# Performance work log

Measured on AMD Instinct MI355X. Metric: run time of the kernel, lower is better.

## Reference

```python
import jax, jax.numpy as jnp
import numpy as np

N_NODES = 100000
N_EDGES = 3200000
D_IN = 256
D_OUT = 256


def setup_inputs() -> dict:
    key = jax.random.key(0)
    k1, k2, k3, k4, k5 = jax.random.split(key, 5)
    X = jax.random.normal(k1, (N_NODES, D_IN), dtype=jnp.float32)
    A_rows = jax.random.randint(k2, (N_EDGES,), 0, N_NODES, dtype=jnp.int64)
    A_cols = jax.random.randint(k3, (N_EDGES,), 0, N_NODES, dtype=jnp.int64)
    A_vals = jax.random.uniform(k4, (N_EDGES,), dtype=jnp.float32)
    # Xavier-uniform init of nn.Linear(in_dim, out_dim, bias=False): W is [out, in]
    limit = float(np.sqrt(6.0 / (D_IN + D_OUT)))
    W = jax.random.uniform(k5, (D_OUT, D_IN), minval=-limit, maxval=limit,
                           dtype=jnp.float32)
    return {"X": X, "A_rows": A_rows, "A_cols": A_cols, "A_vals": A_vals, "W": W}


def reference(X, A_rows, A_cols, A_vals, W):
    # AX = A_coo @ X : gather source features, scale by edge value, scatter-add by row
    msgs = X[A_cols] * A_vals[:, None]                  # [E, D_in]
    AX = jax.ops.segment_sum(msgs, A_rows, num_segments=N_NODES)  # [N, D_in]
    # Linear (bias=False) then ReLU; dropout p=0.0 is identity
    H = jax.nn.relu(AX @ W.T)                           # [N, D_out]
    return H
```

## Files before the change

### kernel.cpp

```cpp
#include <hip/hip_runtime.h>
#include <hip/hip_bf16.h>

#define N_NODES 100000
#define N_EDGES 3200000
#define D 256
#define SHIFT 9
#define NB 196
#define EPB 4096
#define NSPLIT 782
#define NGEMM 1563

typedef __attribute__((ext_vector_type(8))) short short8;
typedef __attribute__((ext_vector_type(4))) float f32x4;

__device__ inline short bfbits(float x) {
    __hip_bfloat16 h = __float2bfloat16(x);
    return __builtin_bit_cast(short, h);
}

__device__ inline short8 load_cvt8(const float* __restrict__ p) {
    float4 a = *(const float4*)p;
    float4 b = *(const float4*)(p + 4);
    short8 r;
    r[0] = bfbits(a.x); r[1] = bfbits(a.y); r[2] = bfbits(a.z); r[3] = bfbits(a.w);
    r[4] = bfbits(b.x); r[5] = bfbits(b.y); r[6] = bfbits(b.z); r[7] = bfbits(b.w);
    return r;
}

__device__ inline int block_excl_scan_256(int c, int* wsum, int& total) {
    const int lane = threadIdx.x & 63, wid = threadIdx.x >> 6;
    int v = c;
    #pragma unroll
    for (int off = 1; off < 64; off <<= 1) {
        int u = __shfl_up(v, off);
        if (lane >= off) v += u;
    }
    if (lane == 63) wsum[wid] = v;
    __syncthreads();
    int w0 = wsum[0], w1 = wsum[1], w2 = wsum[2], w3 = wsum[3];
    total = w0 + w1 + w2 + w3;
    int wex = (wid > 0 ? w0 : 0) + (wid > 1 ? w1 : 0) + (wid > 2 ? w2 : 0);
    return wex + v - c;
}

__global__ __launch_bounds__(256) void bucket_hist(
    const int* __restrict__ rows, int* __restrict__ gcnt, int nE)
{
    __shared__ int h[NB];
    for (int i = threadIdx.x; i < NB; i += 256) h[i] = 0;
    __syncthreads();
    for (int e = blockIdx.x * 256 + threadIdx.x; e < nE; e += gridDim.x * 256)
        atomicAdd(&h[rows[e] >> SHIFT], 1);
    __syncthreads();
    for (int i = threadIdx.x; i < NB; i += 256)
        if (h[i]) atomicAdd(&gcnt[i], h[i]);
}

__global__ __launch_bounds__(256) void bucket_scan(
    const int* __restrict__ gcnt, int* __restrict__ bbase,
    int* __restrict__ gcursor, int* __restrict__ row_ptr)
{
    __shared__ int wsum[4];
    int c = (threadIdx.x < NB) ? gcnt[threadIdx.x] : 0;
    int total;
    int ex = block_excl_scan_256(c, wsum, total);
    if (threadIdx.x < NB) { bbase[threadIdx.x] = ex; gcursor[threadIdx.x] = ex; }
    if (threadIdx.x == 0) { bbase[NB] = total; row_ptr[N_NODES] = total; }
}

__global__ __launch_bounds__(256) void split_gemm(
    const int* __restrict__ rows, const int* __restrict__ cols,
    const float* __restrict__ vals, int* __restrict__ gcursor,
    int2* __restrict__ bcv,
    const float* __restrict__ X, const float* __restrict__ W,
    unsigned short* __restrict__ Y, int nE)
{
    if (blockIdx.x < NSPLIT) {
        __shared__ int cnt[256];
        __shared__ int posp[256];
        const int t  = threadIdx.x;
        const int e0 = blockIdx.x * EPB;

        cnt[t] = 0;
        __syncthreads();

        int  myb[16];
        int2 mycv[16];
        #pragma unroll
        for (int k = 0; k < 16; ++k) {
            int e = e0 + k * 256 + t;
            if (e < nE) {
                int r = rows[e];
                myb[k]  = r >> SHIFT;
                mycv[k] = make_int2(((r & 511) << 17) | cols[e],
                                    __float_as_int(vals[e]));
                atomicAdd(&cnt[myb[k]], 1);
            } else {
                myb[k] = -1;
            }
        }
        __syncthreads();
        if (t < NB) {
            int c = cnt[t];
            posp[t] = c ? atomicAdd(&gcursor[t], c) : 0;
        }
        __syncthreads();
        #pragma unroll
        for (int k = 0; k < 16; ++k) {
            if (myb[k] >= 0) {
                int p = atomicAdd(&posp[myb[k]], 1);
                bcv[p] = mycv[k];
            }
        }
    } else {
        const int bid  = blockIdx.x - NSPLIT;
        const int wid  = threadIdx.x >> 6;
        const int lane = threadIdx.x & 63;
        const int m0   = bid * 64;
        const int n0   = wid * 64;
        const int lr   = lane & 15;
        const int ko   = (lane >> 4) * 8;
        const int M    = N_NODES;

        f32x4 acc[4][4] = {};

        #pragma unroll
        for (int k0 = 0; k0 < 256; k0 += 32) {
            short8 bfrag[4], afrag[4];
            #pragma unroll
            for (int j = 0; j < 4; ++j)
                bfrag[j] = load_cvt8(W + (size_t)(n0 + j * 16 + lr) * 256 + k0 + ko);
            #pragma unroll
            for (int i = 0; i < 4; ++i) {
                int r = m0 + i * 16 + lr;
                if (r > M - 1) r = M - 1;
                afrag[i] = load_cvt8(X + (size_t)r * 256 + k0 + ko);
            }
            #pragma unroll
            for (int i = 0; i < 4; ++i)
                #pragma unroll
                for (int j = 0; j < 4; ++j)
                    acc[i][j] = __builtin_amdgcn_mfma_f32_16x16x32_bf16(
                        afrag[i], bfrag[j], acc[i][j], 0, 0, 0);
        }

        #pragma unroll
        for (int i = 0; i < 4; ++i) {
            int rbase = m0 + i * 16 + (lane >> 4) * 4;
            #pragma unroll
            for (int rr = 0; rr < 4; ++rr) {
                int r = rbase + rr;
                if (r < M) {
                    #pragma unroll
                    for (int j = 0; j < 4; ++j)
                        Y[(size_t)r * 256 + n0 + j * 16 + lr] =
                            (unsigned short)bfbits(acc[i][j][rr]);
                }
            }
        }
    }
}

__global__ __launch_bounds__(256) void bucket_to_csr(
    const int* __restrict__ bbase, const int2* __restrict__ bcv,
    int* __restrict__ row_ptr, int2* __restrict__ cedge)
{
    __shared__ int hist[512];
    __shared__ int cur[512];
    __shared__ int wsum[4];
    const int t  = threadIdx.x;
    const int b  = blockIdx.x;
    const int r0 = b << SHIFT;
    const int s  = bbase[b], e = bbase[b + 1];

    hist[t] = 0; hist[t + 256] = 0;
    __syncthreads();
    for (int j = s + t; j < e; j += 256)
        atomicAdd(&hist[(unsigned)bcv[j].x >> 17], 1);
    __syncthreads();

    int c0 = hist[2 * t], c1 = hist[2 * t + 1];
    int total;
    int ex = block_excl_scan_256(c0 + c1, wsum, total);
    cur[2 * t]     = s + ex;
    cur[2 * t + 1] = s + ex + c0;
    int r = r0 + 2 * t;
    if (r     < N_NODES) row_ptr[r]     = s + ex;
    if (r + 1 < N_NODES) row_ptr[r + 1] = s + ex + c0;
    __syncthreads();

    for (int j = s + t; j < e; j += 256) {
        int2 q = bcv[j];
        int rl = (unsigned)q.x >> 17;
        int p = atomicAdd(&cur[rl], 1);
        cedge[p] = make_int2(q.x & 0x1FFFF, q.y);
    }
}

__global__ __launch_bounds__(256) void spmm_gather_relu(
    const unsigned short* __restrict__ Y,
    const int* __restrict__ row_ptr,
    const int2* __restrict__ cedge,
    float* __restrict__ H)
{
    int row  = blockIdx.x * 4 + (threadIdx.x >> 6);
    int lane = threadIdx.x & 63;
    if (row >= N_NODES) return;
    int s = row_ptr[row];
    int e = row_ptr[row + 1];

    float4 acc = make_float4(0.f, 0.f, 0.f, 0.f);
    const int fo = lane * 4;

    for (int base = s; base < e; base += 64) {
        int idx = base + lane;
        int2 q = make_int2(0, 0);
        if (idx < e) q = cedge[idx];
        int cnt = min(64, e - base);
        int j = 0;
        for (; j + 4 <= cnt; j += 4) {
            int c0 = __builtin_amdgcn_readfirstlane(__shfl(q.x, j));
            int c1 = __builtin_amdgcn_readfirstlane(__shfl(q.x, j + 1));
            int c2 = __builtin_amdgcn_readfirstlane(__shfl(q.x, j + 2));
            int c3 = __builtin_amdgcn_readfirstlane(__shfl(q.x, j + 3));
            float v0 = __int_as_float(__builtin_amdgcn_readfirstlane(__shfl(q.y, j)));
            float v1 = __int_as_float(__builtin_amdgcn_readfirstlane(__shfl(q.y, j + 1)));
            float v2 = __int_as_float(__builtin_amdgcn_readfirstlane(__shfl(q.y, j + 2)));
            float v3 = __int_as_float(__builtin_amdgcn_readfirstlane(__shfl(q.y, j + 3)));
            ushort4 y0 = *(const ushort4*)(Y + (size_t)c0 * 256 + fo);
            ushort4 y1 = *(const ushort4*)(Y + (size_t)c1 * 256 + fo);
            ushort4 y2 = *(const ushort4*)(Y + (size_t)c2 * 256 + fo);
            ushort4 y3 = *(const ushort4*)(Y + (size_t)c3 * 256 + fo);
            acc.x += __uint_as_float((unsigned)y0.x << 16) * v0;
            acc.y += __uint_as_float((unsigned)y0.y << 16) * v0;
            acc.z += __uint_as_float((unsigned)y0.z << 16) * v0;
            acc.w += __uint_as_float((unsigned)y0.w << 16) * v0;
            acc.x += __uint_as_float((unsigned)y1.x << 16) * v1;
            acc.y += __uint_as_float((unsigned)y1.y << 16) * v1;
            acc.z += __uint_as_float((unsigned)y1.z << 16) * v1;
            acc.w += __uint_as_float((unsigned)y1.w << 16) * v1;
            acc.x += __uint_as_float((unsigned)y2.x << 16) * v2;
            acc.y += __uint_as_float((unsigned)y2.y << 16) * v2;
            acc.z += __uint_as_float((unsigned)y2.z << 16) * v2;
            acc.w += __uint_as_float((unsigned)y2.w << 16) * v2;
            acc.x += __uint_as_float((unsigned)y3.x << 16) * v3;
            acc.y += __uint_as_float((unsigned)y3.y << 16) * v3;
            acc.z += __uint_as_float((unsigned)y3.z << 16) * v3;
            acc.w += __uint_as_float((unsigned)y3.w << 16) * v3;
        }
        for (; j < cnt; ++j) {
            int   cj = __builtin_amdgcn_readfirstlane(__shfl(q.x, j));
            float vj = __int_as_float(__builtin_amdgcn_readfirstlane(__shfl(q.y, j)));
            ushort4 y4 = *(const ushort4*)(Y + (size_t)cj * 256 + fo);
            acc.x += __uint_as_float((unsigned)y4.x << 16) * vj;
            acc.y += __uint_as_float((unsigned)y4.y << 16) * vj;
            acc.z += __uint_as_float((unsigned)y4.z << 16) * vj;
            acc.w += __uint_as_float((unsigned)y4.w << 16) * vj;
        }
    }
    float4 r;
    r.x = acc.x > 0.f ? acc.x : 0.f;
    r.y = acc.y > 0.f ? acc.y : 0.f;
    r.z = acc.z > 0.f ? acc.z : 0.f;
    r.w = acc.w > 0.f ? acc.w : 0.f;
    ((float4*)(H + (size_t)row * 256))[lane] = r;
}


extern "C" void kernel_launch(void* const* d_in, const int* in_sizes, int n_in,
                              void* d_out, int out_size, void* d_ws, size_t ws_size,
                              hipStream_t stream) {
    const float* X    = (const float*)d_in[0];
    const int*   rows = (const int*)d_in[1];
    const int*   cols = (const int*)d_in[2];
    const float* vals = (const float*)d_in[3];
    const float* W    = (const float*)d_in[4];
    float*       H    = (float*)d_out;

    char* ws = (char*)d_ws;
    unsigned short* Y       = (unsigned short*)(ws);
    int*            row_ptr = (int*)(ws + 51200000);
    int2*           cedge   = (int2*)(ws + 51600896);
    int2*           bcv     = (int2*)(ws + 77200896);
    int*            gcnt    = (int*)(ws + 102800896);
    int*            bbase   = (int*)(ws + 102801920);
    int*            gcursor = (int*)(ws + 102802944);

    hipMemsetAsync(gcnt, 0, NB * sizeof(int), stream);

    bucket_hist<<<256, 256, 0, stream>>>(rows, gcnt, N_EDGES);
    bucket_scan<<<1, 256, 0, stream>>>(gcnt, bbase, gcursor, row_ptr);
    split_gemm<<<NSPLIT + NGEMM, 256, 0, stream>>>(
        rows, cols, vals, gcursor, bcv, X, W, Y, N_EDGES);
    bucket_to_csr<<<NB, 256, 0, stream>>>(bbase, bcv, row_ptr, cedge);

    spmm_gather_relu<<<(N_NODES + 3) / 4, 256, 0, stream>>>(Y, row_ptr, cedge, H);
}
```

Measured before the change: 456.9 us.

## Replace histogram pass with fixed-capacity buckets and fuse CSR build into GEMM

New measurement: 411.0 us. 10.0% less time.

```diff
diff --git a/kernel.cpp b/kernel.cpp
--- a/kernel.cpp
+++ b/kernel.cpp
@@ -5,7 +5,8 @@
 #define N_EDGES 3200000
 #define D 256
 #define SHIFT 9
-#define NB 196
+#define NBC 196
+#define CAP 18000
 #define EPB 4096
 #define NSPLIT 782
 #define NGEMM 1563
@@ -43,77 +44,119 @@
     return wex + v - c;
 }
 
-__global__ __launch_bounds__(256) void bucket_hist(
-    const int* __restrict__ rows, int* __restrict__ gcnt, int nE)
-{
-    __shared__ int h[NB];
-    for (int i = threadIdx.x; i < NB; i += 256) h[i] = 0;
-    __syncthreads();
-    for (int e = blockIdx.x * 256 + threadIdx.x; e < nE; e += gridDim.x * 256)
-        atomicAdd(&h[rows[e] >> SHIFT], 1);
-    __syncthreads();
-    for (int i = threadIdx.x; i < NB; i += 256)
-        if (h[i]) atomicAdd(&gcnt[i], h[i]);
-}
-
-__global__ __launch_bounds__(256) void bucket_scan(
-    const int* __restrict__ gcnt, int* __restrict__ bbase,
-    int* __restrict__ gcursor, int* __restrict__ row_ptr)
-{
+__global__ __launch_bounds__(256) void init_cursor(int* __restrict__ gcursor)
+{
+    int t = threadIdx.x;
+    if (t < NBC) gcursor[t] = t * CAP;
+}
+
+__global__ __launch_bounds__(256) void bucket_split(
+    const int* __restrict__ rows, const int* __restrict__ cols,
+    const float* __restrict__ vals, int* __restrict__ gcursor,
+    int2* __restrict__ bcv, int nE)
+{
+    __shared__ int cnt[256];
+    __shared__ int startp[256];
+    __shared__ int posp[256];
+    __shared__ int gb[256];
     __shared__ int wsum[4];
-    int c = (threadIdx.x < NB) ? gcnt[threadIdx.x] : 0;
+    __shared__ int2 scv[EPB];
+    const int t  = threadIdx.x;
+    const int e0 = blockIdx.x * EPB;
+
+    cnt[t] = 0;
+    __syncthreads();
+
+    int  myb[16];
+    int2 mycv[16];
+    #pragma unroll
+    for (int k = 0; k < 16; ++k) {
+        int e = e0 + k * 256 + t;
+        if (e < nE) {
+            int r = rows[e];
+            myb[k]  = r >> SHIFT;
+            mycv[k] = make_int2(((r & 511) << 17) | cols[e],
+                                __float_as_int(vals[e]));
+            atomicAdd(&cnt[myb[k]], 1);
+        } else {
+            myb[k] = -1;
+        }
+    }
+    __syncthreads();
+
+    int c = cnt[t];
     int total;
     int ex = block_excl_scan_256(c, wsum, total);
-    if (threadIdx.x < NB) { bbase[threadIdx.x] = ex; gcursor[threadIdx.x] = ex; }
-    if (threadIdx.x == 0) { bbase[NB] = total; row_ptr[N_NODES] = total; }
-}
-
-__global__ __launch_bounds__(256) void split_gemm(
-    const int* __restrict__ rows, const int* __restrict__ cols,
-    const float* __restrict__ vals, int* __restrict__ gcursor,
-    int2* __restrict__ bcv,
+    startp[t] = ex;
+    posp[t]   = ex;
+    if (t < NBC && c) gb[t] = atomicAdd(&gcursor[t], c);
+    __syncthreads();
+
+    #pragma unroll
+    for (int k = 0; k < 16; ++k) {
+        if (myb[k] >= 0) {
+            int p = atomicAdd(&posp[myb[k]], 1);
+            scv[p] = mycv[k];
+        }
+    }
+    __syncthreads();
+
+    const int lane = t & 63, wid = t >> 6;
+    for (int b = wid; b < NBC; b += 4) {
+        int cb = cnt[b];
+        if (!cb) continue;
+        int st = startp[b], g = gb[b];
+        int lim = (b + 1) * CAP;
+        if (g + cb > lim) cb = lim > g ? lim - g : 0;
+        for (int i = lane; i < cb; i += 64)
+            bcv[g + i] = scv[st + i];
+    }
+}
+
+__global__ __launch_bounds__(256) void csr_gemm(
+    const int* __restrict__ gcursor, const int2* __restrict__ bcv,
+    int* __restrict__ rs, int* __restrict__ re, int2* __restrict__ cedge,
     const float* __restrict__ X, const float* __restrict__ W,
-    unsigned short* __restrict__ Y, int nE)
-{
-    if (blockIdx.x < NSPLIT) {
-        __shared__ int cnt[256];
-        __shared__ int posp[256];
-        const int t  = threadIdx.x;
-        const int e0 = blockIdx.x * EPB;
-
-        cnt[t] = 0;
+    unsigned short* __restrict__ Y)
+{
+    if (blockIdx.x < NBC) {
+        __shared__ int hist[512];
+        __shared__ int cur[512];
+        __shared__ int wsum[4];
+        const int t = threadIdx.x;
+        const int b = blockIdx.x;
+        const int s = b * CAP, e = gcursor[b];
+        const int r0 = b << SHIFT;
+
+        hist[t] = 0; hist[t + 256] = 0;
         __syncthreads();
-
-        int  myb[16];
-        int2 mycv[16];
-        #pragma unroll
-        for (int k = 0; k < 16; ++k) {
-            int e = e0 + k * 256 + t;
-            if (e < nE) {
-                int r = rows[e];
-                myb[k]  = r >> SHIFT;
-                mycv[k] = make_int2(((r & 511) << 17) | cols[e],
-                                    __float_as_int(vals[e]));
-                atomicAdd(&cnt[myb[k]], 1);
-            } else {
-                myb[k] = -1;
-            }
-        }
+        for (int j = s + t; j < e; j += 256)
+            atomicAdd(&hist[(unsigned)bcv[j].x >> 17], 1);
         __syncthreads();
-        if (t < NB) {
-            int c = cnt[t];
-            posp[t] = c ? atomicAdd(&gcursor[t], c) : 0;
+
+        int c0 = hist[2 * t], c1 = hist[2 * t + 1];
+        int total;
+        int ex = block_excl_scan_256(c0 + c1, wsum, total);
+        cur[2 * t]     = s + ex;
+        cur[2 * t + 1] = s + ex + c0;
+        int r = r0 + 2 * t;
+        if (r < N_NODES) {
+            rs[r] = s + ex;
+            re[r] = s + ex + c0;
+        }
+        if (r + 1 < N_NODES) {
+            rs[r + 1] = s + ex + c0;
+            re[r + 1] = s + ex + c0 + c1;
         }
         __syncthreads();
-        #pragma unroll
-        for (int k = 0; k < 16; ++k) {
-            if (myb[k] >= 0) {
-                int p = atomicAdd(&posp[myb[k]], 1);
-                bcv[p] = mycv[k];
-            }
+
+        for (int j = s + t; j < e; j += 256) {
+            int2 q = bcv[j];
+            int p = atomicAdd(&cur[(unsigned)q.x >> 17], 1);
+            cedge[p] = q;
         }
     } else {
-        const int bid  = blockIdx.x - NSPLIT;
+        const int bid  = blockIdx.x - NBC;
         const int wid  = threadIdx.x >> 6;
         const int lane = threadIdx.x & 63;
         const int m0   = bid * 64;
@@ -161,53 +204,17 @@
     }
 }
 
-__global__ __launch_bounds__(256) void bucket_to_csr(
-    const int* __restrict__ bbase, const int2* __restrict__ bcv,
-    int* __restrict__ row_ptr, int2* __restrict__ cedge)
-{
-    __shared__ int hist[512];
-    __shared__ int cur[512];
-    __shared__ int wsum[4];
-    const int t  = threadIdx.x;
-    const int b  = blockIdx.x;
-    const int r0 = b << SHIFT;
-    const int s  = bbase[b], e = bbase[b + 1];
-
-    hist[t] = 0; hist[t + 256] = 0;
-    __syncthreads();
-    for (int j = s + t; j < e; j += 256)
-        atomicAdd(&hist[(unsigned)bcv[j].x >> 17], 1);
-    __syncthreads();
-
-    int c0 = hist[2 * t], c1 = hist[2 * t + 1];
-    int total;
-    int ex = block_excl_scan_256(c0 + c1, wsum, total);
-    cur[2 * t]     = s + ex;
-    cur[2 * t + 1] = s + ex + c0;
-    int r = r0 + 2 * t;
-    if (r     < N_NODES) row_ptr[r]     = s + ex;
-    if (r + 1 < N_NODES) row_ptr[r + 1] = s + ex + c0;
-    __syncthreads();
-
-    for (int j = s + t; j < e; j += 256) {
-        int2 q = bcv[j];
-        int rl = (unsigned)q.x >> 17;
-        int p = atomicAdd(&cur[rl], 1);
-        cedge[p] = make_int2(q.x & 0x1FFFF, q.y);
-    }
-}
-
 __global__ __launch_bounds__(256) void spmm_gather_relu(
     const unsigned short* __restrict__ Y,
-    const int* __restrict__ row_ptr,
+    const int* __restrict__ rs, const int* __restrict__ re,
     const int2* __restrict__ cedge,
     float* __restrict__ H)
 {
     int row  = blockIdx.x * 4 + (threadIdx.x >> 6);
     int lane = threadIdx.x & 63;
     if (row >= N_NODES) return;
-    int s = row_ptr[row];
-    int e = row_ptr[row + 1];
+    int s = rs[row];
+    int e = re[row];
 
     float4 acc = make_float4(0.f, 0.f, 0.f, 0.f);
     const int fo = lane * 4;
@@ -219,10 +226,10 @@
         int cnt = min(64, e - base);
         int j = 0;
         for (; j + 4 <= cnt; j += 4) {
-            int c0 = __builtin_amdgcn_readfirstlane(__shfl(q.x, j));
-            int c1 = __builtin_amdgcn_readfirstlane(__shfl(q.x, j + 1));
-            int c2 = __builtin_amdgcn_readfirstlane(__shfl(q.x, j + 2));
-            int c3 = __builtin_amdgcn_readfirstlane(__shfl(q.x, j + 3));
+            int c0 = __builtin_amdgcn_readfirstlane(__shfl(q.x, j))     & 0x1FFFF;
+            int c1 = __builtin_amdgcn_readfirstlane(__shfl(q.x, j + 1)) & 0x1FFFF;
+            int c2 = __builtin_amdgcn_readfirstlane(__shfl(q.x, j + 2)) & 0x1FFFF;
+            int c3 = __builtin_amdgcn_readfirstlane(__shfl(q.x, j + 3)) & 0x1FFFF;
             float v0 = __int_as_float(__builtin_amdgcn_readfirstlane(__shfl(q.y, j)));
             float v1 = __int_as_float(__builtin_amdgcn_readfirstlane(__shfl(q.y, j + 1)));
             float v2 = __int_as_float(__builtin_amdgcn_readfirstlane(__shfl(q.y, j + 2)));
@@ -249,7 +256,7 @@
             acc.w += __uint_as_float((unsigned)y3.w << 16) * v3;
         }
         for (; j < cnt; ++j) {
-            int   cj = __builtin_amdgcn_readfirstlane(__shfl(q.x, j));
+            int   cj = __builtin_amdgcn_readfirstlane(__shfl(q.x, j)) & 0x1FFFF;
             float vj = __int_as_float(__builtin_amdgcn_readfirstlane(__shfl(q.y, j)));
             ushort4 y4 = *(const ushort4*)(Y + (size_t)cj * 256 + fo);
             acc.x += __uint_as_float((unsigned)y4.x << 16) * vj;
@@ -279,20 +286,14 @@
 
     char* ws = (char*)d_ws;
     unsigned short* Y       = (unsigned short*)(ws);
-    int*            row_ptr = (int*)(ws + 51200000);
-    int2*           cedge   = (int2*)(ws + 51600896);
-    int2*           bcv     = (int2*)(ws + 77200896);
-    int*            gcnt    = (int*)(ws + 102800896);
-    int*            bbase   = (int*)(ws + 102801920);
-    int*            gcursor = (int*)(ws + 102802944);
-
-    hipMemsetAsync(gcnt, 0, NB * sizeof(int), stream);
-
-    bucket_hist<<<256, 256, 0, stream>>>(rows, gcnt, N_EDGES);
-    bucket_scan<<<1, 256, 0, stream>>>(gcnt, bbase, gcursor, row_ptr);
-    split_gemm<<<NSPLIT + NGEMM, 256, 0, stream>>>(
-        rows, cols, vals, gcursor, bcv, X, W, Y, N_EDGES);
-    bucket_to_csr<<<NB, 256, 0, stream>>>(bbase, bcv, row_ptr, cedge);
-
-    spmm_gather_relu<<<(N_NODES + 3) / 4, 256, 0, stream>>>(Y, row_ptr, cedge, H);
-}
+    int2*           bcv     = (int2*)(ws + 51200000);
+    int2*           cedge   = (int2*)(ws + 79424000);
+    int*            rs      = (int*)(ws + 107648000);
+    int*            re      = (int*)(ws + 108048128);
+    int*            gcursor = (int*)(ws + 108448256);
+
+    init_cursor<<<1, 256, 0, stream>>>(gcursor);
+    bucket_split<<<NSPLIT, 256, 0, stream>>>(rows, cols, vals, gcursor, bcv, N_EDGES);
+    csr_gemm<<<NBC + NGEMM, 256, 0, stream>>>(gcursor, bcv, rs, re, cedge, X, W, Y);
+    spmm_gather_relu<<<(N_NODES + 3) / 4, 256, 0, stream>>>(Y, rs, re, cedge, H);
+}
```
